# Kernel optimization log

Measured on AMD Instinct MI355X. Metric: run time of the kernel, lower is better.

## Reference

```python
import jax, jax.numpy as jnp
import numpy as np
import math

DIM = 1024
NHEADS = 8
HEAD_DIM = 128
MAXSEQLEN = 2048
THETA = 10000.0


def _rope_tables():
    # speed = theta ** (-(arange(0, dim, 2) / dim)), t = arange(maxseqlen)
    half = HEAD_DIM // 2
    speed = THETA ** (-(np.arange(0, HEAD_DIM, 2)[:half].astype(np.float32) / HEAD_DIM))
    t = np.arange(MAXSEQLEN, dtype=np.float32)
    freqs = np.outer(t, speed)  # [maxseqlen, head_dim//2]
    return jnp.asarray(np.cos(freqs)), jnp.asarray(np.sin(freqs))


def setup_inputs() -> dict:
    key = jax.random.key(0)
    kx, kqkv, kout = jax.random.split(key, 3)
    B, T = 2, 2048
    hdim = NHEADS * HEAD_DIM
    std = 0.5 * DIM ** (-0.5)
    bound = (3.0 ** 0.5) * std
    x = jax.random.normal(kx, (B, T, DIM), dtype=jnp.float32)
    qkv_proj = jax.random.uniform(kqkv, (3, hdim, DIM), dtype=jnp.float32,
                                  minval=-bound, maxval=bound)
    # nn.Linear(hdim, dim, bias=False) default init: U(-1/sqrt(hdim), 1/sqrt(hdim))
    wb = 1.0 / math.sqrt(hdim)
    w_out = jax.random.uniform(kout, (DIM, hdim), dtype=jnp.float32,
                               minval=-wb, maxval=wb)
    cos, sin = _rope_tables()
    return {"x": x, "qkv_proj": qkv_proj, "w_out": w_out, "cos": cos, "sin": sin}


def _apply_rope(u, cos, sin):
    # u: [B, T, H, D]; rotate adjacent pairs (complex multiply)
    B, T, H, D = u.shape
    u = u.reshape(B, T, H, D // 2, 2)
    c = cos[:T][None, :, None, :]  # [1, T, 1, D//2]
    s = sin[:T][None, :, None, :]
    re = u[..., 0] * c - u[..., 1] * s
    im = u[..., 0] * s + u[..., 1] * c
    return jnp.stack([re, im], axis=-1).reshape(B, T, H, D)


def reference(x, qkv_proj, w_out, cos, sin):
    B, T, D = x.shape
    # fused QKV projection: [B, T, 3, hdim] -> [B, T, 3, H, head_dim]
    qkv = jnp.einsum('btd,ahd->btah', x, qkv_proj)
    qkv = qkv.reshape(B, T, 3, NHEADS, HEAD_DIM)
    q, k, v = qkv[:, :, 0], qkv[:, :, 1], qkv[:, :, 2]
    q = _apply_rope(q, cos, sin)
    k = _apply_rope(k, cos, sin)
    scale = HEAD_DIM ** (-0.5)
    logits = jnp.einsum('btnh,bsnh->bnts', q, k) * scale  # [B, H, T, T]
    causal = jnp.tril(jnp.ones((T, T), dtype=bool))
    masked = jnp.where(causal[None, None], logits, -jnp.inf)
    attn = jax.nn.softmax(masked, axis=-1)
    out = jnp.einsum('bnts,bsnh->btnh', attn, v).reshape(B, T, -1)
    out = out @ w_out.T  # [B, T, dim]
    return out, attn
```

## Files before the change

kernel.cpp:

```cpp
#include <hip/hip_runtime.h>

typedef __attribute__((ext_vector_type(8))) short bf16x8;
typedef __attribute__((ext_vector_type(4))) short bf16x4;
typedef __attribute__((ext_vector_type(4))) float f32x4;

#define MFMA(a, b, c) __builtin_amdgcn_mfma_f32_16x16x32_bf16((a), (b), (c), 0, 0, 0)

__device__ __forceinline__ unsigned short f2bf(float f) {
  unsigned int x = __float_as_uint(f);
  return (unsigned short)((x + 0x7fffu + ((x >> 16) & 1u)) >> 16);
}
__device__ __forceinline__ unsigned int cvtpk(float lo, float hi) {
  unsigned int r;
  asm("v_cvt_pk_bf16_f32 %0, %1, %2" : "=v"(r) : "v"(lo), "v"(hi));
  return r;
}

constexpr int SEQ = 2048;
constexpr int NH = 8;
constexpr int DH = 128;
constexpr int DIM = 1024;
constexpr float SCALE = 0.08838834764831845f;

__global__ __launch_bounds__(256) void k_qkv_rope(
    const float* __restrict__ x, const float* __restrict__ wqkv,
    const float* __restrict__ cosT, const float* __restrict__ sinT,
    unsigned short* __restrict__ q, unsigned short* __restrict__ k,
    unsigned short* __restrict__ vT)
{
  __shared__ __align__(16) unsigned short As[128][40];
  __shared__ __align__(16) unsigned short Bs[128][40];
  const int tid = threadIdx.x;
  const int wave = tid >> 6, lane = tid & 63;
  const int fr = lane & 15, fq = lane >> 4;
  const int fk = fq * 8;
  const int wr = (wave >> 1) * 64, wc = (wave & 1) * 64;
  const int m0 = blockIdx.x * 128, n0 = blockIdx.y * 128;

  f32x4 zero4 = {0.f, 0.f, 0.f, 0.f};
  f32x4 acc[4][4];
  for (int i = 0; i < 4; ++i)
    for (int j = 0; j < 4; ++j) acc[i][j] = zero4;

  for (int kt = 0; kt < 32; ++kt) {
    const int k0 = kt * 32;
    __syncthreads();
#pragma unroll
    for (int j = 0; j < 4; ++j) {
      int f = j * 256 + tid;
      int row = f >> 3, c4 = (f & 7) * 4;
      f32x4 va = *(const f32x4*)(x + (m0 + row) * 1024 + k0 + c4);
      f32x4 vb = *(const f32x4*)(wqkv + (n0 + row) * 1024 + k0 + c4);
      uint2 ua, ub;
      ua.x = cvtpk(va[0], va[1]); ua.y = cvtpk(va[2], va[3]);
      ub.x = cvtpk(vb[0], vb[1]); ub.y = cvtpk(vb[2], vb[3]);
      *(uint2*)&As[row][c4] = ua;
      *(uint2*)&Bs[row][c4] = ub;
    }
    __syncthreads();
    bf16x8 af[4], bfr[4];
#pragma unroll
    for (int mi = 0; mi < 4; ++mi) af[mi] = *(const bf16x8*)&As[wr + mi * 16 + fr][fk];
#pragma unroll
    for (int ni = 0; ni < 4; ++ni) bfr[ni] = *(const bf16x8*)&Bs[wc + ni * 16 + fr][fk];
#pragma unroll
    for (int mi = 0; mi < 4; ++mi)
#pragma unroll
      for (int ni = 0; ni < 4; ++ni)
        acc[mi][ni] = MFMA(af[mi], bfr[ni], acc[mi][ni]);
  }

#pragma unroll
  for (int mi = 0; mi < 4; ++mi)
#pragma unroll
    for (int ni = 0; ni < 4; ++ni)
#pragma unroll
      for (int r = 0; r < 4; ++r) {
        float val = acc[mi][ni][r];
        float other = __shfl_xor(val, 1, 64);
        int m = m0 + wr + mi * 16 + fq * 4 + r;
        int n = n0 + wc + ni * 16 + fr;
        int a = n >> 10, feat = n & 1023;
        int hh = feat >> 7, dh = feat & 127;
        int bi = m >> 11, t = m & 2047;
        if (a == 2) {
          vT[((bi * NH + hh) * DH + dh) * SEQ + t] = f2bf(val);
        } else {
          float c = cosT[t * 64 + (dh >> 1)];
          float s = sinT[t * 64 + (dh >> 1)];
          float o = ((dh & 1) == 0) ? (val * c - other * s) : (other * s + val * c);
          unsigned short* dst = (a == 0) ? q : k;
          dst[((bi * NH + hh) * SEQ + t) * DH + dh] = f2bf(o);
        }
      }
}

__global__ __launch_bounds__(256) void k_attn(
    const unsigned short* __restrict__ q, const unsigned short* __restrict__ k,
    const unsigned short* __restrict__ vT,
    float* __restrict__ attn, unsigned short* __restrict__ heads)
{
  __shared__ __align__(16) unsigned short Kt[64][140];
  __shared__ __align__(16) unsigned short Vt[128][76];
  __shared__ __align__(16) unsigned short Esc[4][16][76];

  const int tid = threadIdx.x;
  const int wave = tid >> 6, lane = tid & 63;
  const int fr = lane & 15, fq = lane >> 4;
  const int fk = fq * 8;
  const int rt = (blockIdx.z == 0) ? (int)blockIdx.x : (31 - (int)blockIdx.x);
  const int row0 = rt * 64;
  const int hh = blockIdx.y, bi = blockIdx.z;
  const int bh = bi * NH + hh;
  const int r0 = row0 + wave * 16;

  const unsigned short* qb = q + bh * SEQ * DH;
  const unsigned short* kb = k + bh * SEQ * DH;
  const unsigned short* vb = vT + bh * DH * SEQ;

  bf16x8 aq[4];
#pragma unroll
  for (int ks = 0; ks < 4; ++ks)
    aq[ks] = *(const bf16x8*)(qb + (r0 + fr) * DH + ks * 32 + fk);

  const int wmax = r0 + 15;
  float rs[4] = {0.f, 0.f, 0.f, 0.f};

  for (int nt = 0; nt <= rt; ++nt) {
    const int c0 = nt * 64;
    __syncthreads();
#pragma unroll
    for (int j = 0; j < 4; ++j) {
      int f = j * 256 + tid;
      int r = f >> 4, c = (f & 15) * 8;
      *(bf16x8*)&Kt[r][c] = *(const bf16x8*)(kb + (c0 + r) * DH + c);
    }
    __syncthreads();
#pragma unroll
    for (int half = 0; half < 4; ++half) {
      int ch = c0 + half * 16;
      if (ch <= wmax) {
        f32x4 s = {0.f, 0.f, 0.f, 0.f};
#pragma unroll
        for (int ks = 0; ks < 4; ++ks) {
          bf16x8 bk = *(const bf16x8*)&Kt[half * 16 + fr][ks * 32 + fk];
          s = MFMA(aq[ks], bk, s);
        }
        int col = ch + fr;
#pragma unroll
        for (int r = 0; r < 4; ++r) {
          int row = r0 + fq * 4 + r;
          if (col <= row) rs[r] += __expf(s[r] * SCALE);
        }
      }
    }
  }

#pragma unroll
  for (int r = 0; r < 4; ++r)
#pragma unroll
    for (int msk = 1; msk < 16; msk <<= 1)
      rs[r] += __shfl_xor(rs[r], msk, 64);

  float inv[4];
#pragma unroll
  for (int r = 0; r < 4; ++r) inv[r] = 1.0f / rs[r];

  f32x4 pv[8];
  {
    f32x4 zero4 = {0.f, 0.f, 0.f, 0.f};
#pragma unroll
    for (int i = 0; i < 8; ++i) pv[i] = zero4;
  }

  for (int nt = 0; nt <= rt; ++nt) {
    const int c0 = nt * 64;
    __syncthreads();
#pragma unroll
    for (int j = 0; j < 4; ++j) {
      int f = j * 256 + tid;
      int r = f >> 4, c = (f & 15) * 8;
      *(bf16x8*)&Kt[r][c] = *(const bf16x8*)(kb + (c0 + r) * DH + c);
      int rv = f >> 3, cv = (f & 7) * 8;
      *(bf16x8*)&Vt[rv][cv] = *(const bf16x8*)(vb + rv * SEQ + c0 + cv);
    }
    __syncthreads();
#pragma unroll
    for (int half = 0; half < 4; ++half) {
      int ch = c0 + half * 16;
      bool live = (ch <= wmax);
      f32x4 s = {0.f, 0.f, 0.f, 0.f};
      if (live) {
#pragma unroll
        for (int ks = 0; ks < 4; ++ks) {
          bf16x8 bk = *(const bf16x8*)&Kt[half * 16 + fr][ks * 32 + fk];
          s = MFMA(aq[ks], bk, s);
        }
      }
      int col = ch + fr;
#pragma unroll
      for (int r = 0; r < 4; ++r) {
        int row = r0 + fq * 4 + r;
        float p = (live && col <= row) ? __expf(s[r] * SCALE) * inv[r] : 0.f;
        attn[((size_t)bh * SEQ + row) * SEQ + col] = p;
        Esc[wave][fq * 4 + r][half * 16 + fr] = f2bf(p);
      }
    }
    bf16x8 ae0 = *(const bf16x8*)&Esc[wave][fr][fk];
    bf16x8 ae1 = *(const bf16x8*)&Esc[wave][fr][32 + fk];
#pragma unroll
    for (int ni = 0; ni < 8; ++ni) {
      bf16x8 bv0 = *(const bf16x8*)&Vt[ni * 16 + fr][fk];
      bf16x8 bv1 = *(const bf16x8*)&Vt[ni * 16 + fr][32 + fk];
      pv[ni] = MFMA(ae0, bv0, pv[ni]);
      pv[ni] = MFMA(ae1, bv1, pv[ni]);
    }
  }

#pragma unroll
  for (int ni = 0; ni < 8; ++ni)
#pragma unroll
    for (int r = 0; r < 4; ++r) {
      int row = r0 + fq * 4 + r;
      int dh = ni * 16 + fr;
      heads[(bi * SEQ + row) * DIM + hh * DH + dh] = f2bf(pv[ni][r]);
    }

  {
    const int zstart = row0 + 64;
    f32x4 z4 = {0.f, 0.f, 0.f, 0.f};
#pragma unroll
    for (int rr = 0; rr < 4; ++rr) {
      int row = r0 + rr * 4 + fq;
      float* dst = attn + ((size_t)bh * SEQ + row) * SEQ;
      for (int c = zstart + fr * 4; c < SEQ; c += 64)
        *(f32x4*)(dst + c) = z4;
    }
  }
}

__global__ __launch_bounds__(256) void k_outproj(
    const unsigned short* __restrict__ heads, const float* __restrict__ wout,
    float* __restrict__ out)
{
  __shared__ __align__(16) unsigned short As[128][40];
  __shared__ __align__(16) unsigned short Bs[128][40];
  const int tid = threadIdx.x;
  const int wave = tid >> 6, lane = tid & 63;
  const int fr = lane & 15, fq = lane >> 4;
  const int fk = fq * 8;
  const int wr = (wave >> 1) * 64, wc = (wave & 1) * 64;
  const int m0 = blockIdx.x * 128, n0 = blockIdx.y * 128;

  f32x4 zero4 = {0.f, 0.f, 0.f, 0.f};
  f32x4 acc[4][4];
  for (int i = 0; i < 4; ++i)
    for (int j = 0; j < 4; ++j) acc[i][j] = zero4;

  for (int kt = 0; kt < 32; ++kt) {
    const int k0 = kt * 32;
    __syncthreads();
#pragma unroll
    for (int j = 0; j < 2; ++j) {
      int f = j * 256 + tid;
      int row = f >> 2, c = (f & 3) * 8;
      *(bf16x8*)&As[row][c] = *(const bf16x8*)(heads + (m0 + row) * 1024 + k0 + c);
    }
#pragma unroll
    for (int j = 0; j < 4; ++j) {
      int f = j * 256 + tid;
      int row = f >> 3, c4 = (f & 7) * 4;
      f32x4 vb = *(const f32x4*)(wout + (n0 + row) * 1024 + k0 + c4);
      uint2 ub;
      ub.x = cvtpk(vb[0], vb[1]); ub.y = cvtpk(vb[2], vb[3]);
      *(uint2*)&Bs[row][c4] = ub;
    }
    __syncthreads();
    bf16x8 af[4], bfr[4];
#pragma unroll
    for (int mi = 0; mi < 4; ++mi) af[mi] = *(const bf16x8*)&As[wr + mi * 16 + fr][fk];
#pragma unroll
    for (int ni = 0; ni < 4; ++ni) bfr[ni] = *(const bf16x8*)&Bs[wc + ni * 16 + fr][fk];
#pragma unroll
    for (int mi = 0; mi < 4; ++mi)
#pragma unroll
      for (int ni = 0; ni < 4; ++ni)
        acc[mi][ni] = MFMA(af[mi], bfr[ni], acc[mi][ni]);
  }

#pragma unroll
  for (int mi = 0; mi < 4; ++mi)
#pragma unroll
    for (int ni = 0; ni < 4; ++ni)
#pragma unroll
      for (int r = 0; r < 4; ++r) {
        int m = m0 + wr + mi * 16 + fq * 4 + r;
        int n = n0 + wc + ni * 16 + fr;
        out[m * 1024 + n] = acc[mi][ni][r];
      }
}

extern "C" void kernel_launch(void* const* d_in, const int* in_sizes, int n_in,
                              void* d_out, int out_size, void* d_ws, size_t ws_size,
                              hipStream_t stream)
{
  const float* x    = (const float*)d_in[0];
  const float* wqkv = (const float*)d_in[1];
  const float* wout = (const float*)d_in[2];
  const float* cosT = (const float*)d_in[3];
  const float* sinT = (const float*)d_in[4];

  float* out  = (float*)d_out;
  float* attn = out + 4194304;
  unsigned short* ws   = (unsigned short*)d_ws;
  unsigned short* q     = ws;
  unsigned short* kk    = ws + 4194304;
  unsigned short* vT    = ws + 8388608;
  unsigned short* heads = ws + 12582912;

  k_qkv_rope<<<dim3(32, 24), 256, 0, stream>>>(x, wqkv, cosT, sinT, q, kk, vT);
  k_attn<<<dim3(32, 8, 2), 256, 0, stream>>>(q, kk, vT, attn, heads);
  k_outproj<<<dim3(32, 8), 256, 0, stream>>>(heads, wout, out);
}
```

Baseline: 219.7 us.

## Pre-cast inputs to bf16 and use direct global-to-LDS loads in GEMMs

Adds a cast kernel that converts x, the QKV weights and the output weights to bf16 once per call. The two projection GEMMs then stage tiles with global_load_lds straight into unpadded LDS instead of loading fp32, converting and storing through registers. The change also raises wave priority around the MFMA blocks in all kernels. In exchange it adds an extra launch and a full read/write pass over the inputs, and the unpadded LDS rows may cause bank conflicts on fragment reads.

```diff
diff --git a/kernel.cpp b/kernel.cpp
--- a/kernel.cpp
+++ b/kernel.cpp
@@ -5,6 +5,10 @@
 typedef __attribute__((ext_vector_type(4))) float f32x4;
 
 #define MFMA(a, b, c) __builtin_amdgcn_mfma_f32_16x16x32_bf16((a), (b), (c), 0, 0, 0)
+#define GLOAD16(g, l)                                                        \
+  __builtin_amdgcn_global_load_lds(                                          \
+      (const __attribute__((address_space(1))) void*)(g),                    \
+      (__attribute__((address_space(3))) void*)(l), 16, 0, 0)
 
 __device__ __forceinline__ unsigned short f2bf(float f) {
   unsigned int x = __float_as_uint(f);
@@ -22,20 +26,48 @@
 constexpr int DIM = 1024;
 constexpr float SCALE = 0.08838834764831845f;
 
+__global__ __launch_bounds__(256) void k_cast(
+    const float* __restrict__ x, const float* __restrict__ wqkv,
+    const float* __restrict__ wout, unsigned short* __restrict__ xbf,
+    unsigned short* __restrict__ qkvbf, unsigned short* __restrict__ woutbf)
+{
+  int i = (blockIdx.x * 256 + threadIdx.x) * 8;
+  const float* src;
+  unsigned short* dst;
+  int off;
+  if (i < 4194304) { src = x; dst = xbf; off = i; }
+  else if (i < 7340032) { src = wqkv; dst = qkvbf; off = i - 4194304; }
+  else { src = wout; dst = woutbf; off = i - 7340032; }
+  f32x4 a = *(const f32x4*)(src + off);
+  f32x4 b = *(const f32x4*)(src + off + 4);
+  uint4 u;
+  u.x = cvtpk(a[0], a[1]); u.y = cvtpk(a[2], a[3]);
+  u.z = cvtpk(b[0], b[1]); u.w = cvtpk(b[2], b[3]);
+  *(uint4*)(dst + off) = u;
+}
+
 __global__ __launch_bounds__(256) void k_qkv_rope(
-    const float* __restrict__ x, const float* __restrict__ wqkv,
+    const unsigned short* __restrict__ xbf, const unsigned short* __restrict__ wbf,
     const float* __restrict__ cosT, const float* __restrict__ sinT,
     unsigned short* __restrict__ q, unsigned short* __restrict__ k,
     unsigned short* __restrict__ vT)
 {
-  __shared__ __align__(16) unsigned short As[128][40];
-  __shared__ __align__(16) unsigned short Bs[128][40];
+  __shared__ __align__(16) unsigned short As[128 * 32];
+  __shared__ __align__(16) unsigned short Bs[128 * 32];
   const int tid = threadIdx.x;
   const int wave = tid >> 6, lane = tid & 63;
   const int fr = lane & 15, fq = lane >> 4;
   const int fk = fq * 8;
   const int wr = (wave >> 1) * 64, wc = (wave & 1) * 64;
   const int m0 = blockIdx.x * 128, n0 = blockIdx.y * 128;
+  const int lrow = lane >> 2, lcol = (lane & 3) * 8;
+
+  const unsigned short* gA0 = xbf + (m0 + wave * 32 + lrow) * 1024 + lcol;
+  const unsigned short* gA1 = gA0 + 16 * 1024;
+  const unsigned short* gB0 = wbf + (n0 + wave * 32 + lrow) * 1024 + lcol;
+  const unsigned short* gB1 = gB0 + 16 * 1024;
+  unsigned short* lA = &As[wave * 32 * 32];
+  unsigned short* lB = &Bs[wave * 32 * 32];
 
   f32x4 zero4 = {0.f, 0.f, 0.f, 0.f};
   f32x4 acc[4][4];
@@ -44,30 +76,24 @@
 
   for (int kt = 0; kt < 32; ++kt) {
     const int k0 = kt * 32;
-    __syncthreads();
-#pragma unroll
-    for (int j = 0; j < 4; ++j) {
-      int f = j * 256 + tid;
-      int row = f >> 3, c4 = (f & 7) * 4;
-      f32x4 va = *(const f32x4*)(x + (m0 + row) * 1024 + k0 + c4);
-      f32x4 vb = *(const f32x4*)(wqkv + (n0 + row) * 1024 + k0 + c4);
-      uint2 ua, ub;
-      ua.x = cvtpk(va[0], va[1]); ua.y = cvtpk(va[2], va[3]);
-      ub.x = cvtpk(vb[0], vb[1]); ub.y = cvtpk(vb[2], vb[3]);
-      *(uint2*)&As[row][c4] = ua;
-      *(uint2*)&Bs[row][c4] = ub;
-    }
+    GLOAD16(gA0 + k0, lA);
+    GLOAD16(gA1 + k0, lA + 512);
+    GLOAD16(gB0 + k0, lB);
+    GLOAD16(gB1 + k0, lB + 512);
     __syncthreads();
     bf16x8 af[4], bfr[4];
 #pragma unroll
-    for (int mi = 0; mi < 4; ++mi) af[mi] = *(const bf16x8*)&As[wr + mi * 16 + fr][fk];
-#pragma unroll
-    for (int ni = 0; ni < 4; ++ni) bfr[ni] = *(const bf16x8*)&Bs[wc + ni * 16 + fr][fk];
+    for (int mi = 0; mi < 4; ++mi) af[mi] = *(const bf16x8*)&As[(wr + mi * 16 + fr) * 32 + fk];
+#pragma unroll
+    for (int ni = 0; ni < 4; ++ni) bfr[ni] = *(const bf16x8*)&Bs[(wc + ni * 16 + fr) * 32 + fk];
+    __builtin_amdgcn_s_setprio(1);
 #pragma unroll
     for (int mi = 0; mi < 4; ++mi)
 #pragma unroll
       for (int ni = 0; ni < 4; ++ni)
         acc[mi][ni] = MFMA(af[mi], bfr[ni], acc[mi][ni]);
+    __builtin_amdgcn_s_setprio(0);
+    __syncthreads();
   }
 
 #pragma unroll
@@ -141,11 +167,13 @@
       int ch = c0 + half * 16;
       if (ch <= wmax) {
         f32x4 s = {0.f, 0.f, 0.f, 0.f};
+        __builtin_amdgcn_s_setprio(1);
 #pragma unroll
         for (int ks = 0; ks < 4; ++ks) {
           bf16x8 bk = *(const bf16x8*)&Kt[half * 16 + fr][ks * 32 + fk];
           s = MFMA(aq[ks], bk, s);
         }
+        __builtin_amdgcn_s_setprio(0);
         int col = ch + fr;
 #pragma unroll
         for (int r = 0; r < 4; ++r) {
@@ -191,11 +219,13 @@
       bool live = (ch <= wmax);
       f32x4 s = {0.f, 0.f, 0.f, 0.f};
       if (live) {
+        __builtin_amdgcn_s_setprio(1);
 #pragma unroll
         for (int ks = 0; ks < 4; ++ks) {
           bf16x8 bk = *(const bf16x8*)&Kt[half * 16 + fr][ks * 32 + fk];
           s = MFMA(aq[ks], bk, s);
         }
+        __builtin_amdgcn_s_setprio(0);
       }
       int col = ch + fr;
 #pragma unroll
@@ -208,6 +238,7 @@
     }
     bf16x8 ae0 = *(const bf16x8*)&Esc[wave][fr][fk];
     bf16x8 ae1 = *(const bf16x8*)&Esc[wave][fr][32 + fk];
+    __builtin_amdgcn_s_setprio(1);
 #pragma unroll
     for (int ni = 0; ni < 8; ++ni) {
       bf16x8 bv0 = *(const bf16x8*)&Vt[ni * 16 + fr][fk];
@@ -215,6 +246,7 @@
       pv[ni] = MFMA(ae0, bv0, pv[ni]);
       pv[ni] = MFMA(ae1, bv1, pv[ni]);
     }
+    __builtin_amdgcn_s_setprio(0);
   }
 
 #pragma unroll
@@ -240,17 +272,25 @@
 }
 
 __global__ __launch_bounds__(256) void k_outproj(
-    const unsigned short* __restrict__ heads, const float* __restrict__ wout,
+    const unsigned short* __restrict__ heads, const unsigned short* __restrict__ wbf,
     float* __restrict__ out)
 {
-  __shared__ __align__(16) unsigned short As[128][40];
-  __shared__ __align__(16) unsigned short Bs[128][40];
+  __shared__ __align__(16) unsigned short As[128 * 32];
+  __shared__ __align__(16) unsigned short Bs[128 * 32];
   const int tid = threadIdx.x;
   const int wave = tid >> 6, lane = tid & 63;
   const int fr = lane & 15, fq = lane >> 4;
   const int fk = fq * 8;
   const int wr = (wave >> 1) * 64, wc = (wave & 1) * 64;
   const int m0 = blockIdx.x * 128, n0 = blockIdx.y * 128;
+  const int lrow = lane >> 2, lcol = (lane & 3) * 8;
+
+  const unsigned short* gA0 = heads + (m0 + wave * 32 + lrow) * 1024 + lcol;
+  const unsigned short* gA1 = gA0 + 16 * 1024;
+  const unsigned short* gB0 = wbf + (n0 + wave * 32 + lrow) * 1024 + lcol;
+  const unsigned short* gB1 = gB0 + 16 * 1024;
+  unsigned short* lA = &As[wave * 32 * 32];
+  unsigned short* lB = &Bs[wave * 32 * 32];
 
   f32x4 zero4 = {0.f, 0.f, 0.f, 0.f};
   f32x4 acc[4][4];
@@ -259,33 +299,24 @@
 
   for (int kt = 0; kt < 32; ++kt) {
     const int k0 = kt * 32;
-    __syncthreads();
-#pragma unroll
-    for (int j = 0; j < 2; ++j) {
-      int f = j * 256 + tid;
-      int row = f >> 2, c = (f & 3) * 8;
-      *(bf16x8*)&As[row][c] = *(const bf16x8*)(heads + (m0 + row) * 1024 + k0 + c);
-    }
-#pragma unroll
-    for (int j = 0; j < 4; ++j) {
-      int f = j * 256 + tid;
-      int row = f >> 3, c4 = (f & 7) * 4;
-      f32x4 vb = *(const f32x4*)(wout + (n0 + row) * 1024 + k0 + c4);
-      uint2 ub;
-      ub.x = cvtpk(vb[0], vb[1]); ub.y = cvtpk(vb[2], vb[3]);
-      *(uint2*)&Bs[row][c4] = ub;
-    }
+    GLOAD16(gA0 + k0, lA);
+    GLOAD16(gA1 + k0, lA + 512);
+    GLOAD16(gB0 + k0, lB);
+    GLOAD16(gB1 + k0, lB + 512);
     __syncthreads();
     bf16x8 af[4], bfr[4];
 #pragma unroll
-    for (int mi = 0; mi < 4; ++mi) af[mi] = *(const bf16x8*)&As[wr + mi * 16 + fr][fk];
-#pragma unroll
-    for (int ni = 0; ni < 4; ++ni) bfr[ni] = *(const bf16x8*)&Bs[wc + ni * 16 + fr][fk];
+    for (int mi = 0; mi < 4; ++mi) af[mi] = *(const bf16x8*)&As[(wr + mi * 16 + fr) * 32 + fk];
+#pragma unroll
+    for (int ni = 0; ni < 4; ++ni) bfr[ni] = *(const bf16x8*)&Bs[(wc + ni * 16 + fr) * 32 + fk];
+    __builtin_amdgcn_s_setprio(1);
 #pragma unroll
     for (int mi = 0; mi < 4; ++mi)
 #pragma unroll
       for (int ni = 0; ni < 4; ++ni)
         acc[mi][ni] = MFMA(af[mi], bfr[ni], acc[mi][ni]);
+    __builtin_amdgcn_s_setprio(0);
+    __syncthreads();
   }
 
 #pragma unroll
@@ -312,13 +343,17 @@
 
   float* out  = (float*)d_out;
   float* attn = out + 4194304;
-  unsigned short* ws   = (unsigned short*)d_ws;
-  unsigned short* q     = ws;
-  unsigned short* kk    = ws + 4194304;
-  unsigned short* vT    = ws + 8388608;
-  unsigned short* heads = ws + 12582912;
-
-  k_qkv_rope<<<dim3(32, 24), 256, 0, stream>>>(x, wqkv, cosT, sinT, q, kk, vT);
+  unsigned short* ws = (unsigned short*)d_ws;
+  unsigned short* q      = ws;
+  unsigned short* kk     = ws + 4194304;
+  unsigned short* vT     = ws + 8388608;
+  unsigned short* heads  = ws + 12582912;
+  unsigned short* xbf    = ws + 16777216;
+  unsigned short* qkvbf  = ws + 20971520;
+  unsigned short* woutbf = ws + 24117248;
+
+  k_cast<<<4096, 256, 0, stream>>>(x, wqkv, wout, xbf, qkvbf, woutbf);
+  k_qkv_rope<<<dim3(32, 24), 256, 0, stream>>>(xbf, qkvbf, cosT, sinT, q, kk, vT);
   k_attn<<<dim3(32, 8, 2), 256, 0, stream>>>(q, kk, vT, attn, heads);
-  k_outproj<<<dim3(32, 8), 256, 0, stream>>>(heads, wout, out);
-}
+  k_outproj<<<dim3(32, 8), 256, 0, stream>>>(heads, woutbf, out);
+}
```

After: 253.6 us. +15.4%, slower.

## Load K/V tiles directly from global per wave, drop shared staging and block syncs

Applied to the files above, without the earlier changes.

The attention kernel no longer stages K and V tiles through shared memory behind block-wide barriers. Each wave now loads its own K and V fragments straight from global memory in 32-column chunks, with each wave's causal extent set by its own rows rather than the block's. The change also wraps the MFMA groups in s_setprio and narrows the zero-fill start to per-wave granularity. This removes barrier stalls and the extra LDS round trip, but K and V are now read redundantly by each of the four waves, which raises global/L2 traffic.

```diff
diff --git a/kernel.cpp b/kernel.cpp
--- a/kernel.cpp
+++ b/kernel.cpp
@@ -100,9 +100,7 @@
     const unsigned short* __restrict__ vT,
     float* __restrict__ attn, unsigned short* __restrict__ heads)
 {
-  __shared__ __align__(16) unsigned short Kt[64][140];
-  __shared__ __align__(16) unsigned short Vt[128][76];
-  __shared__ __align__(16) unsigned short Esc[4][16][76];
+  __shared__ __align__(16) unsigned short Esc[4][16][40];
 
   const int tid = threadIdx.x;
   const int wave = tid >> 6, lane = tid & 63;
@@ -124,29 +122,26 @@
     aq[ks] = *(const bf16x8*)(qb + (r0 + fr) * DH + ks * 32 + fk);
 
   const int wmax = r0 + 15;
+  const int nc = r0 >> 5;
+
   float rs[4] = {0.f, 0.f, 0.f, 0.f};
 
-  for (int nt = 0; nt <= rt; ++nt) {
-    const int c0 = nt * 64;
-    __syncthreads();
-#pragma unroll
-    for (int j = 0; j < 4; ++j) {
-      int f = j * 256 + tid;
-      int r = f >> 4, c = (f & 15) * 8;
-      *(bf16x8*)&Kt[r][c] = *(const bf16x8*)(kb + (c0 + r) * DH + c);
-    }
-    __syncthreads();
-#pragma unroll
-    for (int half = 0; half < 4; ++half) {
-      int ch = c0 + half * 16;
+  for (int cc = 0; cc <= nc; ++cc) {
+    const int c0 = cc * 32;
+#pragma unroll
+    for (int half = 0; half < 2; ++half) {
+      const int ch = c0 + half * 16;
       if (ch <= wmax) {
+        bf16x8 bk[4];
+#pragma unroll
+        for (int ks = 0; ks < 4; ++ks)
+          bk[ks] = *(const bf16x8*)(kb + (ch + fr) * DH + ks * 32 + fk);
         f32x4 s = {0.f, 0.f, 0.f, 0.f};
-#pragma unroll
-        for (int ks = 0; ks < 4; ++ks) {
-          bf16x8 bk = *(const bf16x8*)&Kt[half * 16 + fr][ks * 32 + fk];
-          s = MFMA(aq[ks], bk, s);
-        }
-        int col = ch + fr;
+        __builtin_amdgcn_s_setprio(1);
+#pragma unroll
+        for (int ks = 0; ks < 4; ++ks) s = MFMA(aq[ks], bk[ks], s);
+        __builtin_amdgcn_s_setprio(0);
+        const int col = ch + fr;
 #pragma unroll
         for (int r = 0; r < 4; ++r) {
           int row = r0 + fq * 4 + r;
@@ -173,31 +168,29 @@
     for (int i = 0; i < 8; ++i) pv[i] = zero4;
   }
 
-  for (int nt = 0; nt <= rt; ++nt) {
-    const int c0 = nt * 64;
-    __syncthreads();
-#pragma unroll
-    for (int j = 0; j < 4; ++j) {
-      int f = j * 256 + tid;
-      int r = f >> 4, c = (f & 15) * 8;
-      *(bf16x8*)&Kt[r][c] = *(const bf16x8*)(kb + (c0 + r) * DH + c);
-      int rv = f >> 3, cv = (f & 7) * 8;
-      *(bf16x8*)&Vt[rv][cv] = *(const bf16x8*)(vb + rv * SEQ + c0 + cv);
-    }
-    __syncthreads();
-#pragma unroll
-    for (int half = 0; half < 4; ++half) {
-      int ch = c0 + half * 16;
-      bool live = (ch <= wmax);
+  for (int cc = 0; cc <= nc; ++cc) {
+    const int c0 = cc * 32;
+    bf16x8 bv[8];
+#pragma unroll
+    for (int ni = 0; ni < 8; ++ni)
+      bv[ni] = *(const bf16x8*)(vb + (ni * 16 + fr) * SEQ + c0 + fk);
+
+#pragma unroll
+    for (int half = 0; half < 2; ++half) {
+      const int ch = c0 + half * 16;
+      const bool live = (ch <= wmax);
       f32x4 s = {0.f, 0.f, 0.f, 0.f};
       if (live) {
-#pragma unroll
-        for (int ks = 0; ks < 4; ++ks) {
-          bf16x8 bk = *(const bf16x8*)&Kt[half * 16 + fr][ks * 32 + fk];
-          s = MFMA(aq[ks], bk, s);
-        }
-      }
-      int col = ch + fr;
+        bf16x8 bk[4];
+#pragma unroll
+        for (int ks = 0; ks < 4; ++ks)
+          bk[ks] = *(const bf16x8*)(kb + (ch + fr) * DH + ks * 32 + fk);
+        __builtin_amdgcn_s_setprio(1);
+#pragma unroll
+        for (int ks = 0; ks < 4; ++ks) s = MFMA(aq[ks], bk[ks], s);
+        __builtin_amdgcn_s_setprio(0);
+      }
+      const int col = ch + fr;
 #pragma unroll
       for (int r = 0; r < 4; ++r) {
         int row = r0 + fq * 4 + r;
@@ -206,15 +199,11 @@
         Esc[wave][fq * 4 + r][half * 16 + fr] = f2bf(p);
       }
     }
-    bf16x8 ae0 = *(const bf16x8*)&Esc[wave][fr][fk];
-    bf16x8 ae1 = *(const bf16x8*)&Esc[wave][fr][32 + fk];
-#pragma unroll
-    for (int ni = 0; ni < 8; ++ni) {
-      bf16x8 bv0 = *(const bf16x8*)&Vt[ni * 16 + fr][fk];
-      bf16x8 bv1 = *(const bf16x8*)&Vt[ni * 16 + fr][32 + fk];
-      pv[ni] = MFMA(ae0, bv0, pv[ni]);
-      pv[ni] = MFMA(ae1, bv1, pv[ni]);
-    }
+    bf16x8 ae = *(const bf16x8*)&Esc[wave][fr][fk];
+    __builtin_amdgcn_s_setprio(1);
+#pragma unroll
+    for (int ni = 0; ni < 8; ++ni) pv[ni] = MFMA(ae, bv[ni], pv[ni]);
+    __builtin_amdgcn_s_setprio(0);
   }
 
 #pragma unroll
@@ -227,7 +216,7 @@
     }
 
   {
-    const int zstart = row0 + 64;
+    const int zstart = (r0 & ~31) + 32;
     f32x4 z4 = {0.f, 0.f, 0.f, 0.f};
 #pragma unroll
     for (int rr = 0; rr < 4; ++rr) {
@@ -312,7 +301,7 @@
 
   float* out  = (float*)d_out;
   float* attn = out + 4194304;
-  unsigned short* ws   = (unsigned short*)d_ws;
+  unsigned short* ws = (unsigned short*)d_ws;
   unsigned short* q     = ws;
   unsigned short* kk    = ws + 4194304;
   unsigned short* vT    = ws + 8388608;
```

After: 307.7 us. 40.1% more time.

## Double-buffer K tiles via register prefetch and load V directly into registers

Applied to the files above, without the earlier changes.

The attention kernel now keeps two K tiles in shared memory and prefetches the next tile into registers while computing on the current one, so each iteration needs a single barrier instead of two. The second pass walks the tiles in reverse, which lets it reuse the last K tile still resident from the first pass. V is loaded straight from global memory into MFMA operand registers rather than staged through shared memory, and the P·V product is split into two 32-column chunks to shrink the Esc scratch. This is meant to hide global-load latency and cut LDS traffic and synchronisation, at the cost of higher register pressure (16 V fragments plus 4 prefetch registers) and uncoalesced per-lane V loads.

```diff
diff --git a/kernel.cpp b/kernel.cpp
--- a/kernel.cpp
+++ b/kernel.cpp
@@ -100,9 +100,8 @@
     const unsigned short* __restrict__ vT,
     float* __restrict__ attn, unsigned short* __restrict__ heads)
 {
-  __shared__ __align__(16) unsigned short Kt[64][140];
-  __shared__ __align__(16) unsigned short Vt[128][76];
-  __shared__ __align__(16) unsigned short Esc[4][16][76];
+  __shared__ __align__(16) unsigned short Kt[2][64][140];
+  __shared__ __align__(16) unsigned short Esc[4][16][40];
 
   const int tid = threadIdx.x;
   const int wave = tid >> 6, lane = tid & 63;
@@ -123,37 +122,54 @@
   for (int ks = 0; ks < 4; ++ks)
     aq[ks] = *(const bf16x8*)(qb + (r0 + fr) * DH + ks * 32 + fk);
 
+  const int ntiles = rt + 1;
   const int wmax = r0 + 15;
+  const int trow = tid >> 4;
+  const int tcol = (tid & 15) * 8;
+
+  bf16x8 kreg[4];
+#pragma unroll
+  for (int j = 0; j < 4; ++j)
+    kreg[j] = *(const bf16x8*)(kb + (j * 16 + trow) * DH + tcol);
+#pragma unroll
+  for (int j = 0; j < 4; ++j)
+    *(bf16x8*)&Kt[0][j * 16 + trow][tcol] = kreg[j];
+  __syncthreads();
+
+  int cur = 0;
   float rs[4] = {0.f, 0.f, 0.f, 0.f};
 
-  for (int nt = 0; nt <= rt; ++nt) {
+  for (int nt = 0; nt < ntiles; ++nt) {
     const int c0 = nt * 64;
-    __syncthreads();
-#pragma unroll
-    for (int j = 0; j < 4; ++j) {
-      int f = j * 256 + tid;
-      int r = f >> 4, c = (f & 15) * 8;
-      *(bf16x8*)&Kt[r][c] = *(const bf16x8*)(kb + (c0 + r) * DH + c);
-    }
-    __syncthreads();
+    const bool pf = (nt + 1 < ntiles);
+    if (pf) {
+#pragma unroll
+      for (int j = 0; j < 4; ++j)
+        kreg[j] = *(const bf16x8*)(kb + (c0 + 64 + j * 16 + trow) * DH + tcol);
+    }
 #pragma unroll
     for (int half = 0; half < 4; ++half) {
-      int ch = c0 + half * 16;
+      const int ch = c0 + half * 16;
       if (ch <= wmax) {
         f32x4 s = {0.f, 0.f, 0.f, 0.f};
 #pragma unroll
         for (int ks = 0; ks < 4; ++ks) {
-          bf16x8 bk = *(const bf16x8*)&Kt[half * 16 + fr][ks * 32 + fk];
+          bf16x8 bk = *(const bf16x8*)&Kt[cur][half * 16 + fr][ks * 32 + fk];
           s = MFMA(aq[ks], bk, s);
         }
-        int col = ch + fr;
-#pragma unroll
-        for (int r = 0; r < 4; ++r) {
-          int row = r0 + fq * 4 + r;
-          if (col <= row) rs[r] += __expf(s[r] * SCALE);
-        }
+        const int col = ch + fr;
+#pragma unroll
+        for (int r = 0; r < 4; ++r)
+          if (col <= r0 + fq * 4 + r) rs[r] += __expf(s[r] * SCALE);
       }
     }
+    if (pf) {
+#pragma unroll
+      for (int j = 0; j < 4; ++j)
+        *(bf16x8*)&Kt[cur ^ 1][j * 16 + trow][tcol] = kreg[j];
+    }
+    __syncthreads();
+    if (pf) cur ^= 1;
   }
 
 #pragma unroll
@@ -173,48 +189,56 @@
     for (int i = 0; i < 8; ++i) pv[i] = zero4;
   }
 
-  for (int nt = 0; nt <= rt; ++nt) {
+  for (int nt = ntiles - 1; nt >= 0; --nt) {
     const int c0 = nt * 64;
-    __syncthreads();
-#pragma unroll
-    for (int j = 0; j < 4; ++j) {
-      int f = j * 256 + tid;
-      int r = f >> 4, c = (f & 15) * 8;
-      *(bf16x8*)&Kt[r][c] = *(const bf16x8*)(kb + (c0 + r) * DH + c);
-      int rv = f >> 3, cv = (f & 7) * 8;
-      *(bf16x8*)&Vt[rv][cv] = *(const bf16x8*)(vb + rv * SEQ + c0 + cv);
-    }
-    __syncthreads();
-#pragma unroll
-    for (int half = 0; half < 4; ++half) {
-      int ch = c0 + half * 16;
-      bool live = (ch <= wmax);
-      f32x4 s = {0.f, 0.f, 0.f, 0.f};
-      if (live) {
-#pragma unroll
-        for (int ks = 0; ks < 4; ++ks) {
-          bf16x8 bk = *(const bf16x8*)&Kt[half * 16 + fr][ks * 32 + fk];
-          s = MFMA(aq[ks], bk, s);
+    const bool pf = (nt > 0);
+    bf16x8 bv[16];
+#pragma unroll
+    for (int ni = 0; ni < 8; ++ni) {
+      bv[ni]     = *(const bf16x8*)(vb + (ni * 16 + fr) * SEQ + c0 + fk);
+      bv[8 + ni] = *(const bf16x8*)(vb + (ni * 16 + fr) * SEQ + c0 + 32 + fk);
+    }
+    if (pf) {
+#pragma unroll
+      for (int j = 0; j < 4; ++j)
+        kreg[j] = *(const bf16x8*)(kb + (c0 - 64 + j * 16 + trow) * DH + tcol);
+    }
+#pragma unroll
+    for (int chunk = 0; chunk < 2; ++chunk) {
+#pragma unroll
+      for (int h2 = 0; h2 < 2; ++h2) {
+        const int half = chunk * 2 + h2;
+        const int ch = c0 + half * 16;
+        const bool live = (ch <= wmax);
+        f32x4 s = {0.f, 0.f, 0.f, 0.f};
+        if (live) {
+#pragma unroll
+          for (int ks = 0; ks < 4; ++ks) {
+            bf16x8 bk = *(const bf16x8*)&Kt[cur][half * 16 + fr][ks * 32 + fk];
+            s = MFMA(aq[ks], bk, s);
+          }
+        }
+        const int col = ch + fr;
+#pragma unroll
+        for (int r = 0; r < 4; ++r) {
+          int row = r0 + fq * 4 + r;
+          float p = (live && col <= row) ? __expf(s[r] * SCALE) * inv[r] : 0.f;
+          attn[((size_t)bh * SEQ + row) * SEQ + col] = p;
+          Esc[wave][fq * 4 + r][h2 * 16 + fr] = f2bf(p);
         }
       }
-      int col = ch + fr;
-#pragma unroll
-      for (int r = 0; r < 4; ++r) {
-        int row = r0 + fq * 4 + r;
-        float p = (live && col <= row) ? __expf(s[r] * SCALE) * inv[r] : 0.f;
-        attn[((size_t)bh * SEQ + row) * SEQ + col] = p;
-        Esc[wave][fq * 4 + r][half * 16 + fr] = f2bf(p);
-      }
-    }
-    bf16x8 ae0 = *(const bf16x8*)&Esc[wave][fr][fk];
-    bf16x8 ae1 = *(const bf16x8*)&Esc[wave][fr][32 + fk];
-#pragma unroll
-    for (int ni = 0; ni < 8; ++ni) {
-      bf16x8 bv0 = *(const bf16x8*)&Vt[ni * 16 + fr][fk];
-      bf16x8 bv1 = *(const bf16x8*)&Vt[ni * 16 + fr][32 + fk];
-      pv[ni] = MFMA(ae0, bv0, pv[ni]);
-      pv[ni] = MFMA(ae1, bv1, pv[ni]);
-    }
+      bf16x8 ae = *(const bf16x8*)&Esc[wave][fr][fk];
+#pragma unroll
+      for (int ni = 0; ni < 8; ++ni)
+        pv[ni] = MFMA(ae, bv[chunk * 8 + ni], pv[ni]);
+    }
+    if (pf) {
+#pragma unroll
+      for (int j = 0; j < 4; ++j)
+        *(bf16x8*)&Kt[cur ^ 1][j * 16 + trow][tcol] = kreg[j];
+    }
+    __syncthreads();
+    if (pf) cur ^= 1;
   }
 
 #pragma unroll
@@ -312,7 +336,7 @@
 
   float* out  = (float*)d_out;
   float* attn = out + 4194304;
-  unsigned short* ws   = (unsigned short*)d_ws;
+  unsigned short* ws = (unsigned short*)d_ws;
   unsigned short* q     = ws;
   unsigned short* kk    = ws + 4194304;
   unsigned short* vT    = ws + 8388608;
```

Result: slower. 245.5 us (+11.7%).
